# Performance work log

Measured on AMD Instinct MI355X. Metric: run time of the kernel, lower is better.

The kernel has to match this reference:

```python
import jax, jax.numpy as jnp
import numpy as np


def _local_similar(q, k, kH, kW):
    # q, k: [B, C, H, W] -> scores [B, H, W, kH*kW]
    # Matches similar_forward: zero-padded kH x kW neighborhood dot products.
    B, C, H, W = q.shape
    pH, pW = kH // 2, kW // 2
    kp = jnp.pad(k, ((0, 0), (0, 0), (pH, pH), (pW, pW)))
    scores = [
        jnp.einsum('bchw,bchw->bhw', q, kp[:, :, dh:dh + H, dw:dw + W])
        for dh in range(kH) for dw in range(kW)
    ]
    return jnp.stack(scores, axis=-1)


def _local_weighting(v, w, kH, kW):
    # v: [B, C, H, W], w: [B, H, W, kH*kW] -> out [B, C, H, W]
    # Matches weighting_forward: weighted sum over zero-padded neighborhood.
    B, C, H, W = v.shape
    pH, pW = kH // 2, kW // 2
    vp = jnp.pad(v, ((0, 0), (0, 0), (pH, pH), (pW, pW)))
    out = jnp.zeros_like(v)
    idx = 0
    for dh in range(kH):
        for dw in range(kW):
            out = out + w[..., idx][:, None, :, :] * vp[:, :, dh:dh + H, dw:dw + W]
            idx += 1
    return out


def setup_inputs() -> dict:
    key = jax.random.key(0)
    k1, k2, k3, k4 = jax.random.split(key, 4)
    B, C, H, W = 8, 64, 128, 128
    O = 64  # out_channels
    scale = 1.0 / np.sqrt(C).astype(np.float32)
    x = jax.random.normal(k1, (B, C, H, W), jnp.float32)
    W1 = jax.random.normal(k2, (O, C), jnp.float32) * scale  # conv1 (1x1, no bias)
    W2 = jax.random.normal(k3, (O, C), jnp.float32) * scale  # conv2
    W3 = jax.random.normal(k4, (O, C), jnp.float32) * scale  # conv3
    return {"x": x, "W1": W1, "W2": W2, "W3": W3, "kH": 7, "kW": 7}


def reference(x, W1, W2, W3, kH, kW):
    # 1x1 convs == per-pixel channel matmuls
    q = jnp.einsum('oc,bchw->bohw', W1, x)
    k = jnp.einsum('oc,bchw->bohw', W2, x)
    v = jnp.einsum('oc,bchw->bohw', W3, x)
    scores = _local_similar(q, k, kH, kW)          # [B, H, W, kH*kW]
    w = jax.nn.softmax(scores, axis=-1)
    return _local_weighting(v, w, kH, kW)          # [B, O, H, W]
```

## Files before the change

kernel.cpp:

```cpp
#include <hip/hip_runtime.h>
#include <hip/hip_bf16.h>

#define B_ 8
#define C_ 64
#define H_ 128
#define W_ 128
#define HW_ (H_ * W_)

typedef __attribute__((ext_vector_type(8))) _Float16 half8v;
typedef __attribute__((ext_vector_type(4))) float float4v;
typedef _Float16 f16x2 __attribute__((ext_vector_type(2)));

static __device__ inline float dot2(unsigned a, unsigned b, float c) {
    f16x2 ha, hb;
    __builtin_memcpy(&ha, &a, 4);
    __builtin_memcpy(&hb, &b, 4);
#if __has_builtin(__builtin_amdgcn_fdot2)
    return __builtin_amdgcn_fdot2(ha, hb, c, false);
#else
    return fmaf((float)ha.x, (float)hb.x, fmaf((float)ha.y, (float)hb.y, c));
#endif
}

static __device__ inline float2 up2(unsigned u) {
    f16x2 h;
    __builtin_memcpy(&h, &u, 4);
    return make_float2((float)h.x, (float)h.y);
}

#define XG_ 260

__global__ __launch_bounds__(512, 4) void proj_qkv(
    const float* __restrict__ x,
    const float* __restrict__ w1, const float* __restrict__ w2,
    const float* __restrict__ w3,
    _Float16* __restrict__ q, _Float16* __restrict__ k, _Float16* __restrict__ v)
{
    __shared__ float xt[32 * XG_];
    const int b = blockIdx.y;
    const int px0 = blockIdx.x * 128;
    const int t = threadIdx.x;
    const int lane = t & 63;
    const int wave = t >> 6;
    const int wave_m = wave & 1, wave_n = wave >> 1;
    const int n = lane & 15, kg = lane >> 4;

    const float* xb = x + (size_t)b * C_ * HW_;
    #pragma unroll
    for (int r = 0; r < 4; ++r) {
        const int fi = t + r * 512;
        const int pxg = fi & 31;
        const int c = fi >> 5;
        const float4 val = *(const float4*)(xb + (size_t)c * HW_ + px0 + pxg * 4);
        *(float4*)(xt + pxg * XG_ + c * 4) = val;
    }
    __syncthreads();

    float4v acc[3][4];
    #pragma unroll
    for (int tnt = 0; tnt < 3; ++tnt)
        #pragma unroll
        for (int mt = 0; mt < 4; ++mt)
            acc[tnt][mt] = (float4v){0.f, 0.f, 0.f, 0.f};

    const int pxl = wave_m * 64 + n;

    #pragma unroll
    for (int ks = 0; ks < 2; ++ks) {
        half8v ah[4], al[4];
        #pragma unroll
        for (int mt = 0; mt < 4; ++mt) {
            const int px = pxl + mt * 16;
            const float* xp = xt + (px >> 2) * XG_ + (px & 3) + (ks * 32 + kg * 8) * 4;
            #pragma unroll
            for (int j = 0; j < 8; ++j) {
                const float f = xp[j * 4];
                const _Float16 h = (_Float16)f;
                ah[mt][j] = h;
                al[mt][j] = (_Float16)(f - (float)h);
            }
        }
        half8v wfr[3];
        #pragma unroll
        for (int tnt = 0; tnt < 3; ++tnt) {
            const int gnt = wave_n * 3 + tnt;
            const float* wsel = (gnt < 4) ? w1 : (gnt < 8) ? w2 : w3;
            const float* wrow = wsel + ((gnt & 3) * 16 + n) * 64 + ks * 32 + kg * 8;
            const float4 wa = *(const float4*)wrow;
            const float4 wc = *(const float4*)(wrow + 4);
            wfr[tnt][0] = (_Float16)wa.x; wfr[tnt][1] = (_Float16)wa.y;
            wfr[tnt][2] = (_Float16)wa.z; wfr[tnt][3] = (_Float16)wa.w;
            wfr[tnt][4] = (_Float16)wc.x; wfr[tnt][5] = (_Float16)wc.y;
            wfr[tnt][6] = (_Float16)wc.z; wfr[tnt][7] = (_Float16)wc.w;
        }
        #pragma unroll
        for (int tnt = 0; tnt < 3; ++tnt) {
            #pragma unroll
            for (int mt = 0; mt < 4; ++mt) {
                acc[tnt][mt] = __builtin_amdgcn_mfma_f32_16x16x32_f16(
                    wfr[tnt], ah[mt], acc[tnt][mt], 0, 0, 0);
                acc[tnt][mt] = __builtin_amdgcn_mfma_f32_16x16x32_f16(
                    wfr[tnt], al[mt], acc[tnt][mt], 0, 0, 0);
            }
        }
    }

    #pragma unroll
    for (int tnt = 0; tnt < 3; ++tnt) {
        const int gnt = wave_n * 3 + tnt;
        _Float16* base = (gnt < 4) ? q : (gnt < 8) ? k : v;
        const int chunk = gnt & 3;
        #pragma unroll
        for (int mt = 0; mt < 4; ++mt) {
            const int pxm = px0 + wave_m * 64 + mt * 16 + n;
            const float4v d = acc[tnt][mt];
            f16x2 lo = {(_Float16)d[0], (_Float16)d[1]};
            f16x2 hi = {(_Float16)d[2], (_Float16)d[3]};
            uint2 u;
            __builtin_memcpy(&u.x, &lo, 4);
            __builtin_memcpy(&u.y, &hi, 4);
            *(uint2*)(base + (((size_t)b * 4 + chunk) * HW_ + pxm) * 16 + kg * 4) = u;
        }
    }
}

#define HP_ 484
#define PL_ 1948

__global__ __launch_bounds__(512, 4) void local_attn(
    const _Float16* __restrict__ q, const _Float16* __restrict__ k,
    const _Float16* __restrict__ v, float* __restrict__ out)
{
    __shared__ float tile[8 * PL_];
    const int b = blockIdx.z, h0 = blockIdx.y * 16, w0 = blockIdx.x * 16;
    const int t = threadIdx.x;
    const int lane = t & 63, wave = t >> 6;
    const int g = lane & 1;
    const int pixel = wave * 32 + (lane >> 1);
    const int pw = pixel & 15, ph = pixel >> 4;
    const size_t px = (size_t)(h0 + ph) * W_ + (w0 + pw);

    uint4 qv[4];
    #pragma unroll
    for (int pp = 0; pp < 4; ++pp) {
        const int p8 = g * 4 + pp;
        qv[pp] = *(const uint4*)(q + (((size_t)b * 4 + (p8 >> 1)) * HW_ + px) * 16 + (p8 & 1) * 8);
    }

    for (int i = t; i < HP_ * 8; i += 512) {
        const int pix = i >> 3, c8 = i & 7;
        const int r = pix / 22, cl = pix - r * 22;
        const int gh = h0 + r - 3, gw = w0 + cl - 3;
        uint4 val = make_uint4(0u, 0u, 0u, 0u);
        if (gh >= 0 && gh < H_ && gw >= 0 && gw < W_)
            val = *(const uint4*)(k + (((size_t)b * 4 + (c8 >> 1)) * HW_ +
                                       (size_t)gh * W_ + gw) * 16 + (c8 & 1) * 8);
        *(uint4*)(tile + c8 * PL_ + pix * 4) = val;
    }
    __syncthreads();

    uint4 vreg[6];
    #pragma unroll
    for (int r = 0; r < 6; ++r) {
        const int i = t + r * 512;
        const int pix = i >> 3, c8 = i & 7;
        const int rr = pix / 22, cl = pix - rr * 22;
        const int gh = h0 + rr - 3, gw = w0 + cl - 3;
        vreg[r] = make_uint4(0u, 0u, 0u, 0u);
        if (gh >= 0 && gh < H_ && gw >= 0 && gw < W_)
            vreg[r] = *(const uint4*)(v + (((size_t)b * 4 + (c8 >> 1)) * HW_ +
                                           (size_t)gh * W_ + gw) * 16 + (c8 & 1) * 8);
    }

    float sc[49];
    #pragma unroll
    for (int dh = 0; dh < 7; ++dh) {
        #pragma unroll
        for (int dw = 0; dw < 7; ++dw) {
            const int np = ((ph + dh) * 22 + (pw + dw)) * 4;
            float s0 = 0.f, s1 = 0.f, s2 = 0.f, s3 = 0.f;
            #pragma unroll
            for (int pp = 0; pp < 4; ++pp) {
                const uint4 u = *(const uint4*)(tile + (g * 4 + pp) * PL_ + np);
                s0 = dot2(qv[pp].x, u.x, s0);
                s1 = dot2(qv[pp].y, u.y, s1);
                s2 = dot2(qv[pp].z, u.z, s2);
                s3 = dot2(qv[pp].w, u.w, s3);
            }
            sc[dh * 7 + dw] = (s0 + s1) + (s2 + s3);
        }
    }

    #pragma unroll
    for (int i = 0; i < 49; ++i)
        sc[i] += __shfl_xor(sc[i], 1, 64);

    float m = sc[0];
    #pragma unroll
    for (int i = 1; i < 49; ++i) m = fmaxf(m, sc[i]);
    float s = 0.f;
    #pragma unroll
    for (int i = 0; i < 49; ++i) { sc[i] = __expf(sc[i] - m); s += sc[i]; }
    const float inv = 1.f / s;
    #pragma unroll
    for (int i = 0; i < 49; ++i) sc[i] *= inv;

    __syncthreads();

    #pragma unroll
    for (int r = 0; r < 6; ++r) {
        const int i = t + r * 512;
        const int pix = i >> 3, c8 = i & 7;
        *(uint4*)(tile + c8 * PL_ + pix * 4) = vreg[r];
    }
    for (int i = t + 3072; i < HP_ * 8; i += 512) {
        const int pix = i >> 3, c8 = i & 7;
        const int r = pix / 22, cl = pix - r * 22;
        const int gh = h0 + r - 3, gw = w0 + cl - 3;
        uint4 val = make_uint4(0u, 0u, 0u, 0u);
        if (gh >= 0 && gh < H_ && gw >= 0 && gw < W_)
            val = *(const uint4*)(v + (((size_t)b * 4 + (c8 >> 1)) * HW_ +
                                       (size_t)gh * W_ + gw) * 16 + (c8 & 1) * 8);
        *(uint4*)(tile + c8 * PL_ + pix * 4) = val;
    }
    __syncthreads();

    float acc[32];
    #pragma unroll
    for (int c = 0; c < 32; ++c) acc[c] = 0.f;
    #pragma unroll
    for (int dh = 0; dh < 7; ++dh) {
        #pragma unroll
        for (int dw = 0; dw < 7; ++dw) {
            const float wgt = sc[dh * 7 + dw];
            const int np = ((ph + dh) * 22 + (pw + dw)) * 4;
            #pragma unroll
            for (int pp = 0; pp < 4; ++pp) {
                const uint4 u = *(const uint4*)(tile + (g * 4 + pp) * PL_ + np);
                const int a = pp * 8;
                float2 f;
                f = up2(u.x); acc[a + 0] = fmaf(wgt, f.x, acc[a + 0]);
                              acc[a + 1] = fmaf(wgt, f.y, acc[a + 1]);
                f = up2(u.y); acc[a + 2] = fmaf(wgt, f.x, acc[a + 2]);
                              acc[a + 3] = fmaf(wgt, f.y, acc[a + 3]);
                f = up2(u.z); acc[a + 4] = fmaf(wgt, f.x, acc[a + 4]);
                              acc[a + 5] = fmaf(wgt, f.y, acc[a + 5]);
                f = up2(u.w); acc[a + 6] = fmaf(wgt, f.x, acc[a + 6]);
                              acc[a + 7] = fmaf(wgt, f.y, acc[a + 7]);
            }
        }
    }

    #pragma unroll
    for (int pp = 0; pp < 4; ++pp) {
        const int p8 = g * 4 + pp;
        const int ch0 = (p8 >> 1) * 16 + (p8 & 1) * 8;
        #pragma unroll
        for (int j = 0; j < 8; ++j)
            out[((size_t)b * 64 + ch0 + j) * HW_ + px] = acc[pp * 8 + j];
    }
}

extern "C" void kernel_launch(void* const* d_in, const int* in_sizes, int n_in,
                              void* d_out, int out_size, void* d_ws, size_t ws_size,
                              hipStream_t stream) {
    const float* x  = (const float*)d_in[0];
    const float* w1 = (const float*)d_in[1];
    const float* w2 = (const float*)d_in[2];
    const float* w3 = (const float*)d_in[3];

    const size_t NE = (size_t)B_ * 4 * HW_ * 16;
    _Float16* q = (_Float16*)d_ws;
    _Float16* k = q + NE;
    _Float16* v = k + NE;
    float* o = (float*)d_out;

    proj_qkv<<<dim3(HW_ / 128, B_), 512, 0, stream>>>(x, w1, w2, w3, q, k, v);
    local_attn<<<dim3(W_ / 16, H_ / 16, B_), 512, 0, stream>>>(q, k, v, o);
}
```

Before: 141.3 us.

## Fuse QKV projection into local attention kernel with halo recomputation

```diff
diff --git a/kernel.cpp b/kernel.cpp
--- a/kernel.cpp
+++ b/kernel.cpp
@@ -28,108 +28,76 @@
     return make_float2((float)h.x, (float)h.y);
 }
 
-#define XG_ 260
-
-__global__ __launch_bounds__(512, 4) void proj_qkv(
+#define HP_ 484
+#define PL_ 1948
+
+template<bool HALO>
+static __device__ inline void proj_stage(
+    const float* __restrict__ xb, const float* __restrict__ wmat,
+    float* tile, int h0, int w0, int wave, int lane)
+{
+    const int n = lane & 15, kg = lane >> 4;
+    const int NMT = HALO ? 31 : 16;
+    #pragma unroll 1
+    for (int m = wave; m < NMT; m += 8) {
+        const int pxn = m * 16 + n;
+        bool val;
+        size_t gofs;
+        if (HALO) {
+            const int r = pxn / 22, cl = pxn - r * 22;
+            const int gh = h0 + r - 3, gw = w0 + cl - 3;
+            val = (pxn < HP_) && (gh >= 0) && (gh < H_) && (gw >= 0) && (gw < W_);
+            gofs = val ? (size_t)(gh * W_ + gw) : 0;
+        } else {
+            val = true;
+            gofs = (size_t)((h0 + (pxn >> 4)) * W_ + w0 + (pxn & 15));
+        }
+        float4v acc[4];
+        #pragma unroll
+        for (int nt = 0; nt < 4; ++nt) acc[nt] = (float4v){0.f, 0.f, 0.f, 0.f};
+        #pragma unroll
+        for (int ks = 0; ks < 2; ++ks) {
+            half8v ah, al;
+            #pragma unroll
+            for (int j = 0; j < 8; ++j) {
+                const float f = val ? xb[(size_t)(ks * 32 + kg * 8 + j) * HW_ + gofs] : 0.f;
+                const _Float16 h = (_Float16)f;
+                ah[j] = h;
+                al[j] = (_Float16)(f - (float)h);
+            }
+            #pragma unroll
+            for (int nt = 0; nt < 4; ++nt) {
+                const float* wrow = wmat + (nt * 16 + n) * 64 + ks * 32 + kg * 8;
+                const float4 wa = *(const float4*)wrow;
+                const float4 wc = *(const float4*)(wrow + 4);
+                half8v wf;
+                wf[0] = (_Float16)wa.x; wf[1] = (_Float16)wa.y;
+                wf[2] = (_Float16)wa.z; wf[3] = (_Float16)wa.w;
+                wf[4] = (_Float16)wc.x; wf[5] = (_Float16)wc.y;
+                wf[6] = (_Float16)wc.z; wf[7] = (_Float16)wc.w;
+                acc[nt] = __builtin_amdgcn_mfma_f32_16x16x32_f16(wf, ah, acc[nt], 0, 0, 0);
+                acc[nt] = __builtin_amdgcn_mfma_f32_16x16x32_f16(wf, al, acc[nt], 0, 0, 0);
+            }
+        }
+        if (!HALO || pxn < HP_) {
+            #pragma unroll
+            for (int nt = 0; nt < 4; ++nt) {
+                const int c8 = nt * 2 + (kg >> 1);
+                f16x2 lo = {(_Float16)acc[nt][0], (_Float16)acc[nt][1]};
+                f16x2 hi = {(_Float16)acc[nt][2], (_Float16)acc[nt][3]};
+                uint2 u;
+                __builtin_memcpy(&u.x, &lo, 4);
+                __builtin_memcpy(&u.y, &hi, 4);
+                *(uint2*)(tile + c8 * PL_ + pxn * 4 + (kg & 1) * 2) = u;
+            }
+        }
+    }
+}
+
+__global__ __launch_bounds__(512, 4) void fused_attn(
     const float* __restrict__ x,
     const float* __restrict__ w1, const float* __restrict__ w2,
-    const float* __restrict__ w3,
-    _Float16* __restrict__ q, _Float16* __restrict__ k, _Float16* __restrict__ v)
-{
-    __shared__ float xt[32 * XG_];
-    const int b = blockIdx.y;
-    const int px0 = blockIdx.x * 128;
-    const int t = threadIdx.x;
-    const int lane = t & 63;
-    const int wave = t >> 6;
-    const int wave_m = wave & 1, wave_n = wave >> 1;
-    const int n = lane & 15, kg = lane >> 4;
-
-    const float* xb = x + (size_t)b * C_ * HW_;
-    #pragma unroll
-    for (int r = 0; r < 4; ++r) {
-        const int fi = t + r * 512;
-        const int pxg = fi & 31;
-        const int c = fi >> 5;
-        const float4 val = *(const float4*)(xb + (size_t)c * HW_ + px0 + pxg * 4);
-        *(float4*)(xt + pxg * XG_ + c * 4) = val;
-    }
-    __syncthreads();
-
-    float4v acc[3][4];
-    #pragma unroll
-    for (int tnt = 0; tnt < 3; ++tnt)
-        #pragma unroll
-        for (int mt = 0; mt < 4; ++mt)
-            acc[tnt][mt] = (float4v){0.f, 0.f, 0.f, 0.f};
-
-    const int pxl = wave_m * 64 + n;
-
-    #pragma unroll
-    for (int ks = 0; ks < 2; ++ks) {
-        half8v ah[4], al[4];
-        #pragma unroll
-        for (int mt = 0; mt < 4; ++mt) {
-            const int px = pxl + mt * 16;
-            const float* xp = xt + (px >> 2) * XG_ + (px & 3) + (ks * 32 + kg * 8) * 4;
-            #pragma unroll
-            for (int j = 0; j < 8; ++j) {
-                const float f = xp[j * 4];
-                const _Float16 h = (_Float16)f;
-                ah[mt][j] = h;
-                al[mt][j] = (_Float16)(f - (float)h);
-            }
-        }
-        half8v wfr[3];
-        #pragma unroll
-        for (int tnt = 0; tnt < 3; ++tnt) {
-            const int gnt = wave_n * 3 + tnt;
-            const float* wsel = (gnt < 4) ? w1 : (gnt < 8) ? w2 : w3;
-            const float* wrow = wsel + ((gnt & 3) * 16 + n) * 64 + ks * 32 + kg * 8;
-            const float4 wa = *(const float4*)wrow;
-            const float4 wc = *(const float4*)(wrow + 4);
-            wfr[tnt][0] = (_Float16)wa.x; wfr[tnt][1] = (_Float16)wa.y;
-            wfr[tnt][2] = (_Float16)wa.z; wfr[tnt][3] = (_Float16)wa.w;
-            wfr[tnt][4] = (_Float16)wc.x; wfr[tnt][5] = (_Float16)wc.y;
-            wfr[tnt][6] = (_Float16)wc.z; wfr[tnt][7] = (_Float16)wc.w;
-        }
-        #pragma unroll
-        for (int tnt = 0; tnt < 3; ++tnt) {
-            #pragma unroll
-            for (int mt = 0; mt < 4; ++mt) {
-                acc[tnt][mt] = __builtin_amdgcn_mfma_f32_16x16x32_f16(
-                    wfr[tnt], ah[mt], acc[tnt][mt], 0, 0, 0);
-                acc[tnt][mt] = __builtin_amdgcn_mfma_f32_16x16x32_f16(
-                    wfr[tnt], al[mt], acc[tnt][mt], 0, 0, 0);
-            }
-        }
-    }
-
-    #pragma unroll
-    for (int tnt = 0; tnt < 3; ++tnt) {
-        const int gnt = wave_n * 3 + tnt;
-        _Float16* base = (gnt < 4) ? q : (gnt < 8) ? k : v;
-        const int chunk = gnt & 3;
-        #pragma unroll
-        for (int mt = 0; mt < 4; ++mt) {
-            const int pxm = px0 + wave_m * 64 + mt * 16 + n;
-            const float4v d = acc[tnt][mt];
-            f16x2 lo = {(_Float16)d[0], (_Float16)d[1]};
-            f16x2 hi = {(_Float16)d[2], (_Float16)d[3]};
-            uint2 u;
-            __builtin_memcpy(&u.x, &lo, 4);
-            __builtin_memcpy(&u.y, &hi, 4);
-            *(uint2*)(base + (((size_t)b * 4 + chunk) * HW_ + pxm) * 16 + kg * 4) = u;
-        }
-    }
-}
-
-#define HP_ 484
-#define PL_ 1948
-
-__global__ __launch_bounds__(512, 4) void local_attn(
-    const _Float16* __restrict__ q, const _Float16* __restrict__ k,
-    const _Float16* __restrict__ v, float* __restrict__ out)
+    const float* __restrict__ w3, float* __restrict__ out)
 {
     __shared__ float tile[8 * PL_];
     const int b = blockIdx.z, h0 = blockIdx.y * 16, w0 = blockIdx.x * 16;
@@ -139,38 +107,18 @@
     const int pixel = wave * 32 + (lane >> 1);
     const int pw = pixel & 15, ph = pixel >> 4;
     const size_t px = (size_t)(h0 + ph) * W_ + (w0 + pw);
-
+    const float* xb = x + (size_t)b * C_ * HW_;
+
+    proj_stage<false>(xb, w1, tile, h0, w0, wave, lane);
+    __syncthreads();
     uint4 qv[4];
     #pragma unroll
-    for (int pp = 0; pp < 4; ++pp) {
-        const int p8 = g * 4 + pp;
-        qv[pp] = *(const uint4*)(q + (((size_t)b * 4 + (p8 >> 1)) * HW_ + px) * 16 + (p8 & 1) * 8);
-    }
-
-    for (int i = t; i < HP_ * 8; i += 512) {
-        const int pix = i >> 3, c8 = i & 7;
-        const int r = pix / 22, cl = pix - r * 22;
-        const int gh = h0 + r - 3, gw = w0 + cl - 3;
-        uint4 val = make_uint4(0u, 0u, 0u, 0u);
-        if (gh >= 0 && gh < H_ && gw >= 0 && gw < W_)
-            val = *(const uint4*)(k + (((size_t)b * 4 + (c8 >> 1)) * HW_ +
-                                       (size_t)gh * W_ + gw) * 16 + (c8 & 1) * 8);
-        *(uint4*)(tile + c8 * PL_ + pix * 4) = val;
-    }
-    __syncthreads();
-
-    uint4 vreg[6];
-    #pragma unroll
-    for (int r = 0; r < 6; ++r) {
-        const int i = t + r * 512;
-        const int pix = i >> 3, c8 = i & 7;
-        const int rr = pix / 22, cl = pix - rr * 22;
-        const int gh = h0 + rr - 3, gw = w0 + cl - 3;
-        vreg[r] = make_uint4(0u, 0u, 0u, 0u);
-        if (gh >= 0 && gh < H_ && gw >= 0 && gw < W_)
-            vreg[r] = *(const uint4*)(v + (((size_t)b * 4 + (c8 >> 1)) * HW_ +
-                                           (size_t)gh * W_ + gw) * 16 + (c8 & 1) * 8);
-    }
+    for (int pp = 0; pp < 4; ++pp)
+        qv[pp] = *(const uint4*)(tile + (g * 4 + pp) * PL_ + pixel * 4);
+    __syncthreads();
+
+    proj_stage<true>(xb, w2, tile, h0, w0, wave, lane);
+    __syncthreads();
 
     float sc[49];
     #pragma unroll
@@ -207,22 +155,7 @@
 
     __syncthreads();
 
-    #pragma unroll
-    for (int r = 0; r < 6; ++r) {
-        const int i = t + r * 512;
-        const int pix = i >> 3, c8 = i & 7;
-        *(uint4*)(tile + c8 * PL_ + pix * 4) = vreg[r];
-    }
-    for (int i = t + 3072; i < HP_ * 8; i += 512) {
-        const int pix = i >> 3, c8 = i & 7;
-        const int r = pix / 22, cl = pix - r * 22;
-        const int gh = h0 + r - 3, gw = w0 + cl - 3;
-        uint4 val = make_uint4(0u, 0u, 0u, 0u);
-        if (gh >= 0 && gh < H_ && gw >= 0 && gw < W_)
-            val = *(const uint4*)(v + (((size_t)b * 4 + (c8 >> 1)) * HW_ +
-                                       (size_t)gh * W_ + gw) * 16 + (c8 & 1) * 8);
-        *(uint4*)(tile + c8 * PL_ + pix * 4) = val;
-    }
+    proj_stage<true>(xb, w3, tile, h0, w0, wave, lane);
     __syncthreads();
 
     float acc[32];
@@ -268,13 +201,7 @@
     const float* w1 = (const float*)d_in[1];
     const float* w2 = (const float*)d_in[2];
     const float* w3 = (const float*)d_in[3];
-
-    const size_t NE = (size_t)B_ * 4 * HW_ * 16;
-    _Float16* q = (_Float16*)d_ws;
-    _Float16* k = q + NE;
-    _Float16* v = k + NE;
     float* o = (float*)d_out;
 
-    proj_qkv<<<dim3(HW_ / 128, B_), 512, 0, stream>>>(x, w1, w2, w3, q, k, v);
-    local_attn<<<dim3(W_ / 16, H_ / 16, B_), 512, 0, stream>>>(q, k, v, o);
-}
+    fused_attn<<<dim3(W_ / 16, H_ / 16, B_), 512, 0, stream>>>(x, w1, w2, w3, o);
+}
```

Result: slower. 160.8 us (+13.8%).
